# Kernel tuning notes

Hardware: AMD Instinct MI355X
Metric: run time of the kernel (lower is better)

The kernel has to match this reference:

```python
import jax, jax.numpy as jnp
import numpy as np

B, N, H, OUT, VOCAB = 1024, 128, 64, 128, 117


def setup_inputs() -> dict:
    key = jax.random.key(0)
    k_g, k_a, k_e, k1, k2, k3 = jax.random.split(key, 6)
    graph = jax.random.randint(k_g, (B, N), 0, VOCAB, dtype=jnp.int64 if jax.config.jax_enable_x64 else jnp.int32)
    adj = jax.random.uniform(k_a, (B, N, N), dtype=jnp.float32)
    # learned params: embedding table + per-layer GraphLinear weights (torch Linear: [out,in], no bias)
    embed = jax.random.normal(k_e, (VOCAB, H), dtype=jnp.float32) * 0.02
    s = 1.0 / np.sqrt(H)
    W1 = jax.random.uniform(k1, (H, H), minval=-s, maxval=s, dtype=jnp.float32)
    W2 = jax.random.uniform(k2, (H, H), minval=-s, maxval=s, dtype=jnp.float32)
    W3 = jax.random.uniform(k3, (OUT, H), minval=-s, maxval=s, dtype=jnp.float32)
    return {"graph": graph, "adj": adj, "embed": embed, "W1": W1, "W2": W2, "W3": W3}


def reference(graph, adj, embed, W1, W2, W3):
    # h: [B, N, H] atom embeddings
    h = embed[graph]
    weights = (W1, W2, W3)
    n_layers = len(weights)
    for i, W in enumerate(weights):
        # message passing: adj @ h, then per-node linear (no bias): x @ W^T
        h = jnp.einsum('bij,bjd->bid', adj, h)
        h = jnp.einsum('bnd,od->bno', h, W)
        if i < n_layers - 1:
            h = jax.nn.relu(h)
    # sum readout over atoms -> [B, OUT]
    return jnp.sum(h, axis=1)
```

## Files before the change

kernel.cpp:

```cpp
#include <hip/hip_runtime.h>

typedef __bf16 bf16x8 __attribute__((ext_vector_type(8)));
typedef float  f32x4  __attribute__((ext_vector_type(4)));

#define NB 1024
#define NN 128
#define NH 64
#define NOUT 128

__device__ __forceinline__ unsigned short f2b(float f) {
    return __builtin_bit_cast(unsigned short, (__bf16)f);
}

__global__ __launch_bounds__(256, 4)
void rsgcn_fused(const int* __restrict__ graph, const float* __restrict__ adj,
                 const float* __restrict__ embed, const float* __restrict__ W1,
                 const float* __restrict__ W2, const float* __restrict__ W3,
                 float* __restrict__ out)
{
    __shared__ __align__(16) char smem[32768];
    char* const hT_s = smem;
    char* const S_s  = smem + 16384;
    float* const svecp = (float*)S_s;
    float* const svec  = (float*)(S_s + 1024);

    const int b    = blockIdx.x;
    const int t    = threadIdx.x;
    const int lane = t & 63;
    const int wv   = t >> 6;
    const int l15  = lane & 15;
    const int lg   = lane >> 4;

    const float* adjb = adj + (size_t)b * (NN * NN);
    float4 av[16];
    #pragma unroll
    for (int kk = 0; kk < 4; ++kk)
        #pragma unroll
        for (int nt = 0; nt < 2; ++nt)
            #pragma unroll
            for (int h = 0; h < 2; ++h) {
                int row = wv * 32 + nt * 16 + l15;
                int col = kk * 32 + lg * 8 + h * 4;
                av[(kk * 2 + nt) * 2 + h] = *(const float4*)(adjb + row * NN + col);
            }

    {
        const int jq = t & 31;
        const int d0 = (t >> 5) * 8;
        const int4 g4 = *(const int4*)(graph + b * NN + jq * 4);
        float ea[4][8];
        *(float4*)&ea[0][0] = *(const float4*)(embed + g4.x * NH + d0);
        *(float4*)&ea[0][4] = *(const float4*)(embed + g4.x * NH + d0 + 4);
        *(float4*)&ea[1][0] = *(const float4*)(embed + g4.y * NH + d0);
        *(float4*)&ea[1][4] = *(const float4*)(embed + g4.y * NH + d0 + 4);
        *(float4*)&ea[2][0] = *(const float4*)(embed + g4.z * NH + d0);
        *(float4*)&ea[2][4] = *(const float4*)(embed + g4.z * NH + d0 + 4);
        *(float4*)&ea[3][0] = *(const float4*)(embed + g4.w * NH + d0);
        *(float4*)&ea[3][4] = *(const float4*)(embed + g4.w * NH + d0 + 4);
        #pragma unroll
        for (int k = 0; k < 8; ++k) {
            int d = d0 + k;
            ushort4 u;
            u.x = f2b(ea[0][k]); u.y = f2b(ea[1][k]);
            u.z = f2b(ea[2][k]); u.w = f2b(ea[3][k]);
            *(ushort4*)(hT_s + d * 256 + ((jq * 8) ^ ((d & 7) << 4))) = u;
        }
    }

    bf16x8 af[4][2];
    #pragma unroll
    for (int kk = 0; kk < 4; ++kk)
        #pragma unroll
        for (int nt = 0; nt < 2; ++nt) {
            float4 v0 = av[(kk * 2 + nt) * 2 + 0];
            float4 v1 = av[(kk * 2 + nt) * 2 + 1];
            bf16x8 a;
            a[0] = (__bf16)v0.x; a[1] = (__bf16)v0.y; a[2] = (__bf16)v0.z; a[3] = (__bf16)v0.w;
            a[4] = (__bf16)v1.x; a[5] = (__bf16)v1.y; a[6] = (__bf16)v1.z; a[7] = (__bf16)v1.w;
            af[kk][nt] = a;
        }
    __syncthreads();

    #pragma unroll
    for (int layer = 0; layer < 2; ++layer) {
        const float* W = layer ? W2 : W1;

        {
            f32x4 acc[4][2] = {};
            #pragma unroll
            for (int kk = 0; kk < 4; ++kk) {
                bf16x8 ha[4];
                #pragma unroll
                for (int dt = 0; dt < 4; ++dt) {
                    int r = dt * 16 + l15;
                    ha[dt] = *(const bf16x8*)(hT_s + r * 256 + ((kk * 64 + lg * 16) ^ ((r & 7) << 4)));
                }
                #pragma unroll
                for (int nt = 0; nt < 2; ++nt)
                    #pragma unroll
                    for (int dt = 0; dt < 4; ++dt)
                        acc[dt][nt] = __builtin_amdgcn_mfma_f32_16x16x32_bf16(
                            ha[dt], af[kk][nt], acc[dt][nt], 0, 0, 0);
            }
            #pragma unroll
            for (int dt = 0; dt < 4; ++dt)
                #pragma unroll
                for (int nt = 0; nt < 2; ++nt) {
                    int node = wv * 32 + nt * 16 + l15;
                    int dd0  = dt * 16 + lg * 4;
                    ushort4 u;
                    u.x = f2b(acc[dt][nt][0]); u.y = f2b(acc[dt][nt][1]);
                    u.z = f2b(acc[dt][nt][2]); u.w = f2b(acc[dt][nt][3]);
                    *(ushort4*)(S_s + node * 128 + ((dd0 * 2) ^ ((node & 7) << 4))) = u;
                }
        }
        __syncthreads();

        {
            f32x4 acc2[2][4] = {};
            #pragma unroll
            for (int k2 = 0; k2 < 2; ++k2) {
                bf16x8 wf[4];
                #pragma unroll
                for (int dt = 0; dt < 4; ++dt) {
                    const float4* p = (const float4*)(W + (dt * 16 + l15) * NH + k2 * 32 + lg * 8);
                    float4 v0 = p[0], v1 = p[1];
                    bf16x8 a;
                    a[0] = (__bf16)v0.x; a[1] = (__bf16)v0.y; a[2] = (__bf16)v0.z; a[3] = (__bf16)v0.w;
                    a[4] = (__bf16)v1.x; a[5] = (__bf16)v1.y; a[6] = (__bf16)v1.z; a[7] = (__bf16)v1.w;
                    wf[dt] = a;
                }
                #pragma unroll
                for (int nt = 0; nt < 2; ++nt) {
                    int row = wv * 32 + nt * 16 + l15;
                    bf16x8 sa = *(const bf16x8*)(S_s + row * 128 + ((k2 * 64 + lg * 16) ^ ((row & 7) << 4)));
                    #pragma unroll
                    for (int dt = 0; dt < 4; ++dt)
                        acc2[nt][dt] = __builtin_amdgcn_mfma_f32_16x16x32_bf16(
                            sa, wf[dt], acc2[nt][dt], 0, 0, 0);
                }
            }
            #pragma unroll
            for (int nt = 0; nt < 2; ++nt)
                #pragma unroll
                for (int dt = 0; dt < 4; ++dt) {
                    int dout  = dt * 16 + l15;
                    int node0 = wv * 32 + nt * 16 + lg * 4;
                    ushort4 u;
                    u.x = f2b(fmaxf(acc2[nt][dt][0], 0.f));
                    u.y = f2b(fmaxf(acc2[nt][dt][1], 0.f));
                    u.z = f2b(fmaxf(acc2[nt][dt][2], 0.f));
                    u.w = f2b(fmaxf(acc2[nt][dt][3], 0.f));
                    *(ushort4*)(hT_s + dout * 256 + ((node0 * 2) ^ ((dout & 7) << 4))) = u;
                }
        }
        __syncthreads();
    }

    {
        f32x4 acc3[4][2] = {};
        #pragma unroll
        for (int kk = 0; kk < 4; ++kk) {
            bf16x8 ha[4];
            #pragma unroll
            for (int dt = 0; dt < 4; ++dt) {
                int r = dt * 16 + l15;
                ha[dt] = *(const bf16x8*)(hT_s + r * 256 + ((kk * 64 + lg * 16) ^ ((r & 7) << 4)));
            }
            #pragma unroll
            for (int nt = 0; nt < 2; ++nt)
                #pragma unroll
                for (int dt = 0; dt < 4; ++dt)
                    acc3[dt][nt] = __builtin_amdgcn_mfma_f32_16x16x32_bf16(
                        ha[dt], af[kk][nt], acc3[dt][nt], 0, 0, 0);
        }
        float s[4][4];
        #pragma unroll
        for (int dt = 0; dt < 4; ++dt)
            #pragma unroll
            for (int i = 0; i < 4; ++i)
                s[dt][i] = acc3[dt][0][i] + acc3[dt][1][i];
        #pragma unroll
        for (int m = 1; m <= 8; m <<= 1)
            #pragma unroll
            for (int dt = 0; dt < 4; ++dt)
                #pragma unroll
                for (int i = 0; i < 4; ++i)
                    s[dt][i] += __shfl_xor(s[dt][i], m);
        if (l15 == 0) {
            #pragma unroll
            for (int dt = 0; dt < 4; ++dt) {
                f32x4 sv = {s[dt][0], s[dt][1], s[dt][2], s[dt][3]};
                *(f32x4*)(svecp + wv * 64 + dt * 16 + lg * 4) = sv;
            }
        }
    }
    __syncthreads();

    if (t < 64) svec[t] = (svecp[t] + svecp[64 + t]) + (svecp[128 + t] + svecp[192 + t]);
    __syncthreads();

    if (t < 128) {
        const float4* wrow = (const float4*)(W3 + t * NH);
        float a0 = 0.f, a1 = 0.f;
        #pragma unroll
        for (int q = 0; q < 16; q += 2) {
            float4 w0 = wrow[q], w1 = wrow[q + 1];
            a0 += w0.x*svec[q*4+0] + w0.y*svec[q*4+1] + w0.z*svec[q*4+2] + w0.w*svec[q*4+3];
            a1 += w1.x*svec[q*4+4] + w1.y*svec[q*4+5] + w1.z*svec[q*4+6] + w1.w*svec[q*4+7];
        }
        out[b * NOUT + t] = a0 + a1;
    }
}

extern "C" void kernel_launch(void* const* d_in, const int* in_sizes, int n_in,
                              void* d_out, int out_size, void* d_ws, size_t ws_size,
                              hipStream_t stream) {
    const int*   graph = (const int*)d_in[0];
    const float* adjp  = (const float*)d_in[1];
    const float* embed = (const float*)d_in[2];
    const float* W1    = (const float*)d_in[3];
    const float* W2    = (const float*)d_in[4];
    const float* W3    = (const float*)d_in[5];
    float* outp = (float*)d_out;

    rsgcn_fused<<<dim3(NB), dim3(256), 0, stream>>>(graph, adjp, embed, W1, W2, W3, outp);
}
```

Before: 38.93 us.

## Double-buffer hidden-state LDS tile to drop intra-layer barrier and hoist weight loads

```diff
diff --git a/kernel.cpp b/kernel.cpp
--- a/kernel.cpp
+++ b/kernel.cpp
@@ -12,15 +12,16 @@
     return __builtin_bit_cast(unsigned short, (__bf16)f);
 }
 
-__global__ __launch_bounds__(256, 4)
+__global__ __launch_bounds__(256, 3)
 void rsgcn_fused(const int* __restrict__ graph, const float* __restrict__ adj,
                  const float* __restrict__ embed, const float* __restrict__ W1,
                  const float* __restrict__ W2, const float* __restrict__ W3,
                  float* __restrict__ out)
 {
-    __shared__ __align__(16) char smem[32768];
-    char* const hT_s = smem;
-    char* const S_s  = smem + 16384;
+    __shared__ __align__(16) char smem[49152];
+    char* const hT0 = smem;
+    char* const hT1 = smem + 16384;
+    char* const S_s = smem + 32768;
     float* const svecp = (float*)S_s;
     float* const svec  = (float*)(S_s + 1024);
 
@@ -31,6 +32,10 @@
     const int l15  = lane & 15;
     const int lg   = lane >> 4;
 
+    const int jq = t & 31;
+    const int d0 = (t >> 5) * 8;
+    const int4 g4 = *(const int4*)(graph + b * NN + jq * 4);
+
     const float* adjb = adj + (size_t)b * (NN * NN);
     float4 av[16];
     #pragma unroll
@@ -38,34 +43,20 @@
         #pragma unroll
         for (int nt = 0; nt < 2; ++nt)
             #pragma unroll
-            for (int h = 0; h < 2; ++h) {
-                int row = wv * 32 + nt * 16 + l15;
-                int col = kk * 32 + lg * 8 + h * 4;
-                av[(kk * 2 + nt) * 2 + h] = *(const float4*)(adjb + row * NN + col);
-            }
-
-    {
-        const int jq = t & 31;
-        const int d0 = (t >> 5) * 8;
-        const int4 g4 = *(const int4*)(graph + b * NN + jq * 4);
-        float ea[4][8];
-        *(float4*)&ea[0][0] = *(const float4*)(embed + g4.x * NH + d0);
-        *(float4*)&ea[0][4] = *(const float4*)(embed + g4.x * NH + d0 + 4);
-        *(float4*)&ea[1][0] = *(const float4*)(embed + g4.y * NH + d0);
-        *(float4*)&ea[1][4] = *(const float4*)(embed + g4.y * NH + d0 + 4);
-        *(float4*)&ea[2][0] = *(const float4*)(embed + g4.z * NH + d0);
-        *(float4*)&ea[2][4] = *(const float4*)(embed + g4.z * NH + d0 + 4);
-        *(float4*)&ea[3][0] = *(const float4*)(embed + g4.w * NH + d0);
-        *(float4*)&ea[3][4] = *(const float4*)(embed + g4.w * NH + d0 + 4);
-        #pragma unroll
-        for (int k = 0; k < 8; ++k) {
-            int d = d0 + k;
-            ushort4 u;
-            u.x = f2b(ea[0][k]); u.y = f2b(ea[1][k]);
-            u.z = f2b(ea[2][k]); u.w = f2b(ea[3][k]);
-            *(ushort4*)(hT_s + d * 256 + ((jq * 8) ^ ((d & 7) << 4))) = u;
-        }
-    }
+            for (int h = 0; h < 2; ++h)
+                av[(kk * 2 + nt) * 2 + h] =
+                    *(const float4*)(adjb + (wv * 32 + nt * 16 + l15) * NN
+                                     + kk * 32 + lg * 8 + h * 4);
+
+    float ea[4][8];
+    *(float4*)&ea[0][0] = *(const float4*)(embed + g4.x * NH + d0);
+    *(float4*)&ea[0][4] = *(const float4*)(embed + g4.x * NH + d0 + 4);
+    *(float4*)&ea[1][0] = *(const float4*)(embed + g4.y * NH + d0);
+    *(float4*)&ea[1][4] = *(const float4*)(embed + g4.y * NH + d0 + 4);
+    *(float4*)&ea[2][0] = *(const float4*)(embed + g4.z * NH + d0);
+    *(float4*)&ea[2][4] = *(const float4*)(embed + g4.z * NH + d0 + 4);
+    *(float4*)&ea[3][0] = *(const float4*)(embed + g4.w * NH + d0);
+    *(float4*)&ea[3][4] = *(const float4*)(embed + g4.w * NH + d0 + 4);
 
     bf16x8 af[4][2];
     #pragma unroll
@@ -79,21 +70,47 @@
             a[4] = (__bf16)v1.x; a[5] = (__bf16)v1.y; a[6] = (__bf16)v1.z; a[7] = (__bf16)v1.w;
             af[kk][nt] = a;
         }
+
+    #pragma unroll
+    for (int k = 0; k < 8; ++k) {
+        int d = d0 + k;
+        ushort4 u;
+        u.x = f2b(ea[0][k]); u.y = f2b(ea[1][k]);
+        u.z = f2b(ea[2][k]); u.w = f2b(ea[3][k]);
+        *(ushort4*)(hT0 + d * 256 + ((jq * 8) ^ ((d & 7) << 4))) = u;
+    }
     __syncthreads();
 
+    const char* hTin  = hT0;
+    char*       hTout = hT1;
     #pragma unroll
     for (int layer = 0; layer < 2; ++layer) {
         const float* W = layer ? W2 : W1;
 
+        bf16x8 wf[2][4];
+        #pragma unroll
+        for (int k2 = 0; k2 < 2; ++k2)
+            #pragma unroll
+            for (int dt = 0; dt < 4; ++dt) {
+                const float4* p = (const float4*)(W + (dt * 16 + l15) * NH
+                                                  + k2 * 32 + lg * 8);
+                float4 v0 = p[0], v1 = p[1];
+                bf16x8 a;
+                a[0] = (__bf16)v0.x; a[1] = (__bf16)v0.y; a[2] = (__bf16)v0.z; a[3] = (__bf16)v0.w;
+                a[4] = (__bf16)v1.x; a[5] = (__bf16)v1.y; a[6] = (__bf16)v1.z; a[7] = (__bf16)v1.w;
+                wf[k2][dt] = a;
+            }
+
         {
             f32x4 acc[4][2] = {};
             #pragma unroll
             for (int kk = 0; kk < 4; ++kk) {
+                const int kb = kk * 64 + lg * 16;
                 bf16x8 ha[4];
                 #pragma unroll
                 for (int dt = 0; dt < 4; ++dt) {
                     int r = dt * 16 + l15;
-                    ha[dt] = *(const bf16x8*)(hT_s + r * 256 + ((kk * 64 + lg * 16) ^ ((r & 7) << 4)));
+                    ha[dt] = *(const bf16x8*)(hTin + r * 256 + (kb ^ ((r & 7) << 4)));
                 }
                 #pragma unroll
                 for (int nt = 0; nt < 2; ++nt)
@@ -114,30 +131,21 @@
                     *(ushort4*)(S_s + node * 128 + ((dd0 * 2) ^ ((node & 7) << 4))) = u;
                 }
         }
-        __syncthreads();
+        asm volatile("s_waitcnt lgkmcnt(0)" ::: "memory");
 
         {
             f32x4 acc2[2][4] = {};
             #pragma unroll
             for (int k2 = 0; k2 < 2; ++k2) {
-                bf16x8 wf[4];
-                #pragma unroll
-                for (int dt = 0; dt < 4; ++dt) {
-                    const float4* p = (const float4*)(W + (dt * 16 + l15) * NH + k2 * 32 + lg * 8);
-                    float4 v0 = p[0], v1 = p[1];
-                    bf16x8 a;
-                    a[0] = (__bf16)v0.x; a[1] = (__bf16)v0.y; a[2] = (__bf16)v0.z; a[3] = (__bf16)v0.w;
-                    a[4] = (__bf16)v1.x; a[5] = (__bf16)v1.y; a[6] = (__bf16)v1.z; a[7] = (__bf16)v1.w;
-                    wf[dt] = a;
-                }
+                const int kb = k2 * 64 + lg * 16;
                 #pragma unroll
                 for (int nt = 0; nt < 2; ++nt) {
                     int row = wv * 32 + nt * 16 + l15;
-                    bf16x8 sa = *(const bf16x8*)(S_s + row * 128 + ((k2 * 64 + lg * 16) ^ ((row & 7) << 4)));
+                    bf16x8 sa = *(const bf16x8*)(S_s + row * 128 + (kb ^ ((row & 7) << 4)));
                     #pragma unroll
                     for (int dt = 0; dt < 4; ++dt)
                         acc2[nt][dt] = __builtin_amdgcn_mfma_f32_16x16x32_bf16(
-                            sa, wf[dt], acc2[nt][dt], 0, 0, 0);
+                            sa, wf[k2][dt], acc2[nt][dt], 0, 0, 0);
                 }
             }
             #pragma unroll
@@ -151,21 +159,24 @@
                     u.y = f2b(fmaxf(acc2[nt][dt][1], 0.f));
                     u.z = f2b(fmaxf(acc2[nt][dt][2], 0.f));
                     u.w = f2b(fmaxf(acc2[nt][dt][3], 0.f));
-                    *(ushort4*)(hT_s + dout * 256 + ((node0 * 2) ^ ((dout & 7) << 4))) = u;
+                    *(ushort4*)(hTout + dout * 256 + ((node0 * 2) ^ ((dout & 7) << 4))) = u;
                 }
         }
         __syncthreads();
+
+        const char* tmp = hTin; hTin = hTout; hTout = (char*)tmp;
     }
 
     {
         f32x4 acc3[4][2] = {};
         #pragma unroll
         for (int kk = 0; kk < 4; ++kk) {
+            const int kb = kk * 64 + lg * 16;
             bf16x8 ha[4];
             #pragma unroll
             for (int dt = 0; dt < 4; ++dt) {
                 int r = dt * 16 + l15;
-                ha[dt] = *(const bf16x8*)(hT_s + r * 256 + ((kk * 64 + lg * 16) ^ ((r & 7) << 4)));
+                ha[dt] = *(const bf16x8*)(hTin + r * 256 + (kb ^ ((r & 7) << 4)));
             }
             #pragma unroll
             for (int nt = 0; nt < 2; ++nt)
@@ -174,12 +185,9 @@
                     acc3[dt][nt] = __builtin_amdgcn_mfma_f32_16x16x32_bf16(
                         ha[dt], af[kk][nt], acc3[dt][nt], 0, 0, 0);
         }
-        float s[4][4];
-        #pragma unroll
-        for (int dt = 0; dt < 4; ++dt)
-            #pragma unroll
-            for (int i = 0; i < 4; ++i)
-                s[dt][i] = acc3[dt][0][i] + acc3[dt][1][i];
+        f32x4 s[4];
+        #pragma unroll
+        for (int dt = 0; dt < 4; ++dt) s[dt] = acc3[dt][0] + acc3[dt][1];
         #pragma unroll
         for (int m = 1; m <= 8; m <<= 1)
             #pragma unroll
@@ -189,15 +197,14 @@
                     s[dt][i] += __shfl_xor(s[dt][i], m);
         if (l15 == 0) {
             #pragma unroll
-            for (int dt = 0; dt < 4; ++dt) {
-                f32x4 sv = {s[dt][0], s[dt][1], s[dt][2], s[dt][3]};
-                *(f32x4*)(svecp + wv * 64 + dt * 16 + lg * 4) = sv;
-            }
+            for (int dt = 0; dt < 4; ++dt)
+                *(f32x4*)(svecp + wv * 64 + dt * 16 + lg * 4) = s[dt];
         }
     }
     __syncthreads();
 
-    if (t < 64) svec[t] = (svecp[t] + svecp[64 + t]) + (svecp[128 + t] + svecp[192 + t]);
+    if (t < 64)
+        svec[t] = (svecp[t] + svecp[64 + t]) + (svecp[128 + t] + svecp[192 + t]);
     __syncthreads();
 
     if (t < 128) {
```

Result: faster. 37.11 us (-4.7%).
